# Performance work log

Hardware: AMD Instinct MI355X
Metric: run time of the kernel (lower is better)

Reference implementation:

```python
import jax, jax.numpy as jnp
import numpy as np

B, T, IN, H = 64, 2048, 512, 128
EPS = 1e-5


def mish(x):
    return x * jnp.tanh(jax.nn.softplus(x))


def layernorm(x, g, b):
    m = jnp.mean(x, axis=-1, keepdims=True)
    v = jnp.mean((x - m) ** 2, axis=-1, keepdims=True)
    return (x - m) / jnp.sqrt(v + EPS) * g + b


def gru_dir(x, Wih, Whh, bih, bhh, reverse):
    """One direction of a PyTorch-convention GRU layer.
    x: [B, T, D_in]; Wih: [3H, D_in]; Whh: [3H, H]. Returns ([B,T,H] outputs, [B,H] final h).
    Gate order matches torch: reset, update, new."""
    # Precompute all input projections once (hoists the big GEMM out of the scan)
    xp = jnp.einsum('bti,gi->tbg', x, Wih) + bih  # [T, B, 3H]
    h0 = jnp.zeros((x.shape[0], Whh.shape[1]), x.dtype)

    def step(h, xt):
        gh = h @ Whh.T + bhh
        xr, xz, xn = jnp.split(xt, 3, axis=-1)
        hr, hz, hn = jnp.split(gh, 3, axis=-1)
        r = jax.nn.sigmoid(xr + hr)
        z = jax.nn.sigmoid(xz + hz)
        n = jnp.tanh(xn + r * hn)
        h_new = (1.0 - z) * n + z * h
        return h_new, h_new

    hT, ys = jax.lax.scan(step, h0, xp, reverse=reverse)
    return jnp.transpose(ys, (1, 0, 2)), hT


def setup_inputs() -> dict:
    key = jax.random.key(0)
    ks = iter(jax.random.split(key, 32))
    s = 0.05

    def p(shape):
        return jax.random.normal(next(ks), shape, dtype=jnp.float32) * s

    inp = {'x': jax.random.normal(next(ks), (B, T, IN), dtype=jnp.float32)}
    # GRU layer 0 (input IN), layer 1 (input 2H from bidirectional concat); f/b directions
    for name, din in (('0f', IN), ('0b', IN), ('1f', 2 * H), ('1b', 2 * H)):
        inp['Wih' + name] = p((3 * H, din))
        inp['Whh' + name] = p((3 * H, H))
        inp['bih' + name] = p((3 * H,))
        inp['bhh' + name] = p((3 * H,))
    # post_gru LayerNorm
    inp['g1'] = jnp.ones((H,), jnp.float32)
    inp['be1'] = jnp.zeros((H,), jnp.float32)
    # decoder: Linear(H,H) -> Mish -> LayerNorm -> Linear(H,1)
    inp['W1'] = p((H, H))
    inp['b1'] = p((H,))
    inp['g2'] = jnp.ones((H,), jnp.float32)
    inp['be2'] = jnp.zeros((H,), jnp.float32)
    inp['W2'] = p((1, H))
    inp['b2'] = p((1,))
    return inp


def reference(x, Wih0f, Whh0f, bih0f, bhh0f, Wih0b, Whh0b, bih0b, bhh0b,
              Wih1f, Whh1f, bih1f, bhh1f, Wih1b, Whh1b, bih1b, bhh1b,
              g1, be1, W1, b1, g2, be2, W2, b2):
    # Layer 0, both directions
    of, _ = gru_dir(x, Wih0f, Whh0f, bih0f, bhh0f, reverse=False)
    ob, _ = gru_dir(x, Wih0b, Whh0b, bih0b, bhh0b, reverse=True)
    x1 = jnp.concatenate([of, ob], axis=-1)  # [B, T, 2H]; inter-layer dropout is identity in eval
    # Layer 1; keep final hidden states (h_n)
    _, hf = gru_dir(x1, Wih1f, Whh1f, bih1f, bhh1f, reverse=False)
    _, hb = gru_dir(x1, Wih1b, Whh1b, bih1b, bhh1b, reverse=True)
    h = hb  # h_n[-1]: last layer, backward direction (PyTorch h_n layout) -> [B, H]
    # post_gru: Mish -> LayerNorm -> AlphaDropout(eval=identity)
    h = layernorm(mish(h), g1, be1)
    # decoder: Linear -> Mish -> LayerNorm -> Linear
    h = layernorm(mish(h @ W1.T + b1), g2, be2)
    return h @ W2.T + b2  # [B, 1]
```

## Files before the change

### kernel.cpp

```cpp
#include <hip/hip_runtime.h>
#include <hip/hip_bf16.h>
#include <cstddef>

#define T_SEQ 2048
#define BATCH 64
#define H 128
#define EPS 1e-5f

typedef _Float16 half8_t __attribute__((ext_vector_type(8)));
typedef _Float16 half4_t __attribute__((ext_vector_type(4)));
typedef float floatx4 __attribute__((ext_vector_type(4)));

__device__ __forceinline__ float sigmoid_f(float x) {
    return __builtin_amdgcn_rcpf(1.0f + __expf(-x));
}
__device__ __forceinline__ float tanh_f(float x) {
    return fmaf(2.0f, __builtin_amdgcn_rcpf(1.0f + __expf(-2.0f * x)), -1.0f);
}
__device__ __forceinline__ float mish_f(float x) {
    float sp = (x > 15.0f) ? x : log1pf(__expf(x));
    return x * tanh_f(sp);
}


template<int K>
__global__ __launch_bounds__(256, 2)
void proj_kernel(const float* __restrict__ A, const float* __restrict__ W,
                 const float* __restrict__ bih, const float* __restrict__ bhh,
                 float* __restrict__ C)
{
    __shared__ float As[16][128];
    __shared__ float Ws[16][128];
    const int n0 = blockIdx.x * 128;
    const int m0 = blockIdx.y * 128;
    const int tid = threadIdx.x;
    const int tx = tid & 15;
    const int ty = tid >> 4;
    float acc[8][8];
    #pragma unroll
    for (int i = 0; i < 8; ++i)
        #pragma unroll
        for (int j = 0; j < 8; ++j) acc[i][j] = 0.0f;

    for (int k0 = 0; k0 < K; k0 += 16) {
        #pragma unroll
        for (int i = 0; i < 2; ++i) {
            const int f = tid + i * 256;
            const int r = f >> 2;
            const int kq = (f & 3) << 2;
            const int m = m0 + r;
            const size_t arow = (size_t)(m & 63) * T_SEQ + (m >> 6);
            const float4 av = *reinterpret_cast<const float4*>(&A[arow * K + k0 + kq]);
            As[kq + 0][r] = av.x; As[kq + 1][r] = av.y;
            As[kq + 2][r] = av.z; As[kq + 3][r] = av.w;
            const float4 wv = *reinterpret_cast<const float4*>(&W[(size_t)(n0 + r) * K + k0 + kq]);
            Ws[kq + 0][r] = wv.x; Ws[kq + 1][r] = wv.y;
            Ws[kq + 2][r] = wv.z; Ws[kq + 3][r] = wv.w;
        }
        __syncthreads();
        #pragma unroll
        for (int kk = 0; kk < 16; ++kk) {
            float a[8], b[8];
            *reinterpret_cast<float4*>(&a[0]) = *reinterpret_cast<const float4*>(&As[kk][ty * 8]);
            *reinterpret_cast<float4*>(&a[4]) = *reinterpret_cast<const float4*>(&As[kk][ty * 8 + 4]);
            *reinterpret_cast<float4*>(&b[0]) = *reinterpret_cast<const float4*>(&Ws[kk][tx * 8]);
            *reinterpret_cast<float4*>(&b[4]) = *reinterpret_cast<const float4*>(&Ws[kk][tx * 8 + 4]);
            #pragma unroll
            for (int i = 0; i < 8; ++i)
                #pragma unroll
                for (int j = 0; j < 8; ++j)
                    acc[i][j] = fmaf(a[i], b[j], acc[i][j]);
        }
        __syncthreads();
    }
    float bv[8];
    #pragma unroll
    for (int j = 0; j < 8; ++j) {
        const int col = n0 + tx * 8 + j;
        bv[j] = bih[col] + ((col < 256) ? bhh[col] : 0.0f);
    }
    const int cq0 = (n0 >> 2) + tx * 2;
    #pragma unroll
    for (int i = 0; i < 8; ++i) {
        const int m = m0 + ty * 8 + i;
        const int t = m >> 6, b = m & 63;
        const int gi = b >> 4, ni = b & 15;
        float* base = &C[(((size_t)t * 4 + gi) * 96 + cq0) * 64 + ni * 4];
        float4 o0, o1;
        o0.x = acc[i][0] + bv[0]; o0.y = acc[i][1] + bv[1];
        o0.z = acc[i][2] + bv[2]; o0.w = acc[i][3] + bv[3];
        o1.x = acc[i][4] + bv[4]; o1.y = acc[i][5] + bv[5];
        o1.z = acc[i][6] + bv[6]; o1.w = acc[i][7] + bv[7];
        *reinterpret_cast<float4*>(base) = o0;
        *reinterpret_cast<float4*>(base + 64) = o1;
    }
}

__device__ __forceinline__ int hoff(int n, int k) {
    return (n * 256 + k * 2) ^ ((n & 7) << 4);
}
#define LDS_BARRIER() asm volatile("s_waitcnt lgkmcnt(0)\n\ts_barrier" ::: "memory")

__global__ __launch_bounds__(512, 2)
void gru_scan8(const float* __restrict__ xpA, const float* __restrict__ xpB,
               const float* __restrict__ WA, const float* __restrict__ WB,
               const float* __restrict__ bA, const float* __restrict__ bB,
               int revA, int revB,
               float* __restrict__ seqout,
               float* __restrict__ hfin)
{
    const int tid = threadIdx.x;
    const int w = tid >> 6;
    const int l = tid & 63;
    const int n = l & 15;
    const int q = l >> 4;

    const int cid = blockIdx.x;
    const int dir = cid >> 2;
    const int g = cid & 3;

    const float* __restrict__ xp  = dir ? xpB : xpA;
    const float* __restrict__ Whh = dir ? WB : WA;
    const float* __restrict__ bhh = dir ? bB : bA;
    const int rev = dir ? revB : revA;

    __shared__ __align__(16) unsigned char hlds[2][4096];

    *reinterpret_cast<unsigned long long*>(&hlds[0][tid * 8]) = 0ull;

    half8_t wf[3][4];
    #pragma unroll
    for (int mi = 0; mi < 3; ++mi) {
        const float* wr = &Whh[(size_t)((mi * 8 + w) * 16 + n) * 128 + q * 8];
        #pragma unroll
        for (int kt = 0; kt < 4; ++kt) {
            half8_t hf;
            #pragma unroll
            for (int e = 0; e < 8; ++e) hf[e] = (_Float16)wr[kt * 32 + e];
            wf[mi][kt] = hf;
        }
    }

    const int batch = g * 16 + n;
    const floatx4 bN = *reinterpret_cast<const floatx4*>(&bhh[256 + w * 16 + q * 4]);
    floatx4 hp = {0.f, 0.f, 0.f, 0.f};

    const int t0 = rev ? (T_SEQ - 1) : 0;
    const int ts = rev ? -1 : 1;

    const float* xbase = xp + ((size_t)(g * 96 + w * 4 + q) * 16 + n) * 4;

#define XLOAD(S, T)                                                                 \
    do {                                                                            \
        const float* p_ = xbase + (size_t)(T) * 24576;                              \
        S[0] = *reinterpret_cast<const floatx4*>(p_);                               \
        S[1] = *reinterpret_cast<const floatx4*>(p_ + 2048);                        \
        S[2] = *reinterpret_cast<const floatx4*>(p_ + 4096);                        \
    } while (0)

    floatx4 XA[3], XB[3], XC[3], XD[3];
    XLOAD(XA, t0);
    XLOAD(XB, t0 + ts);
    XLOAD(XC, t0 + 2 * ts);

    __syncthreads();

#define GRU_STEP(RB, WB_, XS, TCUR)                                                 \
    do {                                                                            \
        half8_t bf0 = *reinterpret_cast<const half8_t*>(&hlds[RB][hoff(n, 0 * 32 + q * 8)]); \
        half8_t bf1 = *reinterpret_cast<const half8_t*>(&hlds[RB][hoff(n, 1 * 32 + q * 8)]); \
        half8_t bf2 = *reinterpret_cast<const half8_t*>(&hlds[RB][hoff(n, 2 * 32 + q * 8)]); \
        half8_t bf3 = *reinterpret_cast<const half8_t*>(&hlds[RB][hoff(n, 3 * 32 + q * 8)]); \
        floatx4 a0 = {0.f, 0.f, 0.f, 0.f};                                          \
        floatx4 a1 = {0.f, 0.f, 0.f, 0.f};                                          \
        floatx4 a2 = bN;                                                            \
        a0 = __builtin_amdgcn_mfma_f32_16x16x32_f16(wf[0][0], bf0, a0, 0, 0, 0);    \
        a1 = __builtin_amdgcn_mfma_f32_16x16x32_f16(wf[1][0], bf0, a1, 0, 0, 0);    \
        a2 = __builtin_amdgcn_mfma_f32_16x16x32_f16(wf[2][0], bf0, a2, 0, 0, 0);    \
        a0 = __builtin_amdgcn_mfma_f32_16x16x32_f16(wf[0][1], bf1, a0, 0, 0, 0);    \
        a1 = __builtin_amdgcn_mfma_f32_16x16x32_f16(wf[1][1], bf1, a1, 0, 0, 0);    \
        a2 = __builtin_amdgcn_mfma_f32_16x16x32_f16(wf[2][1], bf1, a2, 0, 0, 0);    \
        a0 = __builtin_amdgcn_mfma_f32_16x16x32_f16(wf[0][2], bf2, a0, 0, 0, 0);    \
        a1 = __builtin_amdgcn_mfma_f32_16x16x32_f16(wf[1][2], bf2, a1, 0, 0, 0);    \
        a2 = __builtin_amdgcn_mfma_f32_16x16x32_f16(wf[2][2], bf2, a2, 0, 0, 0);    \
        a0 = __builtin_amdgcn_mfma_f32_16x16x32_f16(wf[0][3], bf3, a0, 0, 0, 0);    \
        a1 = __builtin_amdgcn_mfma_f32_16x16x32_f16(wf[1][3], bf3, a1, 0, 0, 0);    \
        a2 = __builtin_amdgcn_mfma_f32_16x16x32_f16(wf[2][3], bf3, a2, 0, 0, 0);    \
        floatx4 hnew;                                                               \
        half4_t hh;                                                                 \
        _Pragma("unroll")                                                           \
        for (int rr = 0; rr < 4; ++rr) {                                            \
            const float rg = sigmoid_f(a0[rr] + XS[0][rr]);                         \
            const float zg = sigmoid_f(a1[rr] + XS[1][rr]);                         \
            const float nn = tanh_f(XS[2][rr] + rg * a2[rr]);                       \
            const float hv = fmaf(zg, hp[rr] - nn, nn);                             \
            hnew[rr] = hv;                                                          \
            hh[rr] = (_Float16)hv;                                                  \
        }                                                                           \
        hp = hnew;                                                                  \
        *reinterpret_cast<half4_t*>(&hlds[WB_][hoff(n, w * 16 + q * 4)]) = hh;      \
        if (seqout)                                                                 \
            *reinterpret_cast<floatx4*>(                                            \
                &seqout[((size_t)batch * T_SEQ + (TCUR)) * 256 + dir * 128 +        \
                        w * 16 + q * 4]) = hnew;                                    \
        LDS_BARRIER();                                                              \
    } while (0)

#define CLAMP_T(v) ((v) < 0 ? 0 : ((v) > T_SEQ - 1 ? T_SEQ - 1 : (v)))

    int t = t0;
    for (int it = 0; it < T_SEQ / 4; ++it) {
        { const int tl = CLAMP_T(t + 3 * ts); XLOAD(XD, tl); }
        GRU_STEP(0, 1, XA, t); t += ts;
        { const int tl = CLAMP_T(t + 3 * ts); XLOAD(XA, tl); }
        GRU_STEP(1, 0, XB, t); t += ts;
        { const int tl = CLAMP_T(t + 3 * ts); XLOAD(XB, tl); }
        GRU_STEP(0, 1, XC, t); t += ts;
        { const int tl = CLAMP_T(t + 3 * ts); XLOAD(XC, tl); }
        GRU_STEP(1, 0, XD, t); t += ts;
    }
#undef GRU_STEP
#undef XLOAD
#undef CLAMP_T

    if (hfin)
        *reinterpret_cast<floatx4*>(&hfin[(size_t)batch * 128 + w * 16 + q * 4]) = hp;
}

__device__ __forceinline__ float block_sum128(float v, float* red) {
    #pragma unroll
    for (int o = 32; o > 0; o >>= 1) v += __shfl_down(v, o);
    const int w = threadIdx.x >> 6;
    if ((threadIdx.x & 63) == 0) red[w] = v;
    __syncthreads();
    const float s = red[0] + red[1];
    __syncthreads();
    return s;
}

__global__ __launch_bounds__(128, 1)
void decoder_kernel(const float* __restrict__ hb,
                    const float* __restrict__ g1, const float* __restrict__ be1,
                    const float* __restrict__ W1, const float* __restrict__ b1,
                    const float* __restrict__ g2, const float* __restrict__ be2,
                    const float* __restrict__ W2, const float* __restrict__ b2,
                    float* __restrict__ out)
{
    const int b = blockIdx.x;
    const int j = threadIdx.x;
    __shared__ float buf[H];
    __shared__ float red[2];

    const float m = mish_f(hb[(size_t)b * H + j]);
    const float mean = block_sum128(m, red) * (1.0f / H);
    const float d = m - mean;
    const float var = block_sum128(d * d, red) * (1.0f / H);
    const float y = d * rsqrtf(var + EPS) * g1[j] + be1[j];
    buf[j] = y;
    __syncthreads();

    float acc = b1[j];
    #pragma unroll
    for (int k = 0; k < H; k += 4) {
        const float4 wv = *reinterpret_cast<const float4*>(&W1[(size_t)j * H + k]);
        const float4 yv = *reinterpret_cast<const float4*>(&buf[k]);
        acc += wv.x * yv.x + wv.y * yv.y + wv.z * yv.z + wv.w * yv.w;
    }
    const float m2 = mish_f(acc);
    const float mean2 = block_sum128(m2, red) * (1.0f / H);
    const float d2 = m2 - mean2;
    const float var2 = block_sum128(d2 * d2, red) * (1.0f / H);
    const float y2 = d2 * rsqrtf(var2 + EPS) * g2[j] + be2[j];

    const float p = W2[j] * y2;
    const float s = block_sum128(p, red);
    if (j == 0) out[b] = s + b2[0];
}

extern "C" void kernel_launch(void* const* d_in, const int* in_sizes, int n_in,
                              void* d_out, int out_size, void* d_ws, size_t ws_size,
                              hipStream_t stream)
{
    (void)in_sizes; (void)n_in; (void)out_size; (void)ws_size;
    const float* x     = (const float*)d_in[0];
    const float* Wih0f = (const float*)d_in[1];
    const float* Whh0f = (const float*)d_in[2];
    const float* bih0f = (const float*)d_in[3];
    const float* bhh0f = (const float*)d_in[4];
    const float* Wih0b = (const float*)d_in[5];
    const float* Whh0b = (const float*)d_in[6];
    const float* bih0b = (const float*)d_in[7];
    const float* bhh0b = (const float*)d_in[8];
    const float* Wih1b = (const float*)d_in[13];
    const float* Whh1b = (const float*)d_in[14];
    const float* bih1b = (const float*)d_in[15];
    const float* bhh1b = (const float*)d_in[16];
    const float* g1  = (const float*)d_in[17];
    const float* be1 = (const float*)d_in[18];
    const float* W1  = (const float*)d_in[19];
    const float* b1  = (const float*)d_in[20];
    const float* g2  = (const float*)d_in[21];
    const float* be2 = (const float*)d_in[22];
    const float* W2  = (const float*)d_in[23];
    const float* b2  = (const float*)d_in[24];
    float* out = (float*)d_out;

    float* ws = (float*)d_ws;
    const size_t XP_ELEMS = (size_t)T_SEQ * BATCH * 384;
    const size_t X1_ELEMS = (size_t)BATCH * T_SEQ * 256;
    float* xp0f = ws;
    float* xp0b = xp0f + XP_ELEMS;
    float* x1   = xp0b + XP_ELEMS;
    float* hbuf = x1 + X1_ELEMS;
    float* xp1b = xp0f;

    const dim3 pgrid(3, 1024);
    proj_kernel<512><<<pgrid, 256, 0, stream>>>(x, Wih0f, bih0f, bhh0f, xp0f);
    proj_kernel<512><<<pgrid, 256, 0, stream>>>(x, Wih0b, bih0b, bhh0b, xp0b);
    gru_scan8<<<dim3(8), 512, 0, stream>>>(xp0f, xp0b, Whh0f, Whh0b, bhh0f, bhh0b,
                                           0, 1, x1, nullptr);
    proj_kernel<256><<<pgrid, 256, 0, stream>>>(x1, Wih1b, bih1b, bhh1b, xp1b);
    gru_scan8<<<dim3(4), 512, 0, stream>>>(xp1b, xp1b, Whh1b, Whh1b, bhh1b, bhh1b,
                                           1, 1, nullptr, hbuf);
    decoder_kernel<<<64, 128, 0, stream>>>(hbuf, g1, be1, W1, b1, g2, be2, W2, b2, out);
}
```

Before: 4.896 ms.

## Replace FP32 projection GEMM with FP16 MFMA kernel and double-buffered LDS

Rewrites the input-projection GEMM to convert inputs and weights to fp16 in shared memory and compute with 16x16x32 MFMA instructions, accumulating in fp32. Global loads for the next K tile are issued before the current tile's MFMAs and staged into a second LDS buffer, so memory latency overlaps with compute. This targets the scalar-FMA cost of the three projection GEMMs. The trade-off is reduced input precision, since activations and weights are rounded to fp16 before the multiply.

```diff
diff --git a/kernel.cpp b/kernel.cpp
--- a/kernel.cpp
+++ b/kernel.cpp
@@ -25,74 +25,107 @@
 
 template<int K>
 __global__ __launch_bounds__(256, 2)
-void proj_kernel(const float* __restrict__ A, const float* __restrict__ W,
-                 const float* __restrict__ bih, const float* __restrict__ bhh,
-                 float* __restrict__ C)
+void proj_mfma(const float* __restrict__ A, const float* __restrict__ W,
+               const float* __restrict__ bih, const float* __restrict__ bhh,
+               float* __restrict__ C)
 {
-    __shared__ float As[16][128];
-    __shared__ float Ws[16][128];
+    constexpr int NKT = K / 32;
+    __shared__ _Float16 Ws[2][128][40];
+    __shared__ _Float16 Xs[2][128][40];
+
+    const int tid = threadIdx.x;
+    const int w = tid >> 6, l = tid & 63;
+    const int lm = l & 15, q = l >> 4;
+    const int wm = (w & 1) * 64, wn = (w >> 1) * 64;
     const int n0 = blockIdx.x * 128;
     const int m0 = blockIdx.y * 128;
-    const int tid = threadIdx.x;
-    const int tx = tid & 15;
-    const int ty = tid >> 4;
-    float acc[8][8];
-    #pragma unroll
-    for (int i = 0; i < 8; ++i)
-        #pragma unroll
-        for (int j = 0; j < 8; ++j) acc[i][j] = 0.0f;
-
-    for (int k0 = 0; k0 < K; k0 += 16) {
-        #pragma unroll
-        for (int i = 0; i < 2; ++i) {
-            const int f = tid + i * 256;
-            const int r = f >> 2;
-            const int kq = (f & 3) << 2;
-            const int m = m0 + r;
-            const size_t arow = (size_t)(m & 63) * T_SEQ + (m >> 6);
-            const float4 av = *reinterpret_cast<const float4*>(&A[arow * K + k0 + kq]);
-            As[kq + 0][r] = av.x; As[kq + 1][r] = av.y;
-            As[kq + 2][r] = av.z; As[kq + 3][r] = av.w;
-            const float4 wv = *reinterpret_cast<const float4*>(&W[(size_t)(n0 + r) * K + k0 + kq]);
-            Ws[kq + 0][r] = wv.x; Ws[kq + 1][r] = wv.y;
-            Ws[kq + 2][r] = wv.z; Ws[kq + 3][r] = wv.w;
+
+    const int sr = tid >> 1;
+    const int sk = (tid & 1) * 16;
+    const int sm = m0 + sr;
+    const float* xrow = A + ((size_t)(sm & 63) * T_SEQ + (sm >> 6)) * K + sk;
+    const float* wrow = W + (size_t)(n0 + sr) * K + sk;
+
+    floatx4 acc[4][4];
+    #pragma unroll
+    for (int i = 0; i < 4; ++i)
+        #pragma unroll
+        for (int j = 0; j < 4; ++j) acc[i][j] = floatx4{0.f, 0.f, 0.f, 0.f};
+
+    floatx4 bv[4];
+    #pragma unroll
+    for (int nf = 0; nf < 4; ++nf) {
+        const int nc = n0 + wn + nf * 16 + q * 4;
+        floatx4 b = *reinterpret_cast<const floatx4*>(&bih[nc]);
+        if (nc < 256) b += *reinterpret_cast<const floatx4*>(&bhh[nc]);
+        bv[nf] = b;
+    }
+
+    floatx4 lx[4], lw[4];
+
+#define STORE_STAGE(B)                                                          \
+    do {                                                                        \
+        half8_t h0, h1, g0, g1;                                                 \
+        _Pragma("unroll")                                                       \
+        for (int e = 0; e < 4; ++e) {                                           \
+            h0[e] = (_Float16)lx[0][e]; h0[4 + e] = (_Float16)lx[1][e];         \
+            h1[e] = (_Float16)lx[2][e]; h1[4 + e] = (_Float16)lx[3][e];         \
+            g0[e] = (_Float16)lw[0][e]; g0[4 + e] = (_Float16)lw[1][e];         \
+            g1[e] = (_Float16)lw[2][e]; g1[4 + e] = (_Float16)lw[3][e];         \
+        }                                                                       \
+        *reinterpret_cast<half8_t*>(&Xs[B][sr][sk])     = h0;                   \
+        *reinterpret_cast<half8_t*>(&Xs[B][sr][sk + 8]) = h1;                   \
+        *reinterpret_cast<half8_t*>(&Ws[B][sr][sk])     = g0;                   \
+        *reinterpret_cast<half8_t*>(&Ws[B][sr][sk + 8]) = g1;                   \
+    } while (0)
+
+    #pragma unroll
+    for (int i = 0; i < 4; ++i) {
+        lx[i] = *reinterpret_cast<const floatx4*>(xrow + i * 4);
+        lw[i] = *reinterpret_cast<const floatx4*>(wrow + i * 4);
+    }
+    STORE_STAGE(0);
+    __syncthreads();
+
+    int buf = 0;
+    for (int kt = 0; kt < NKT; ++kt) {
+        if (kt + 1 < NKT) {
+            #pragma unroll
+            for (int i = 0; i < 4; ++i) {
+                lx[i] = *reinterpret_cast<const floatx4*>(xrow + (kt + 1) * 32 + i * 4);
+                lw[i] = *reinterpret_cast<const floatx4*>(wrow + (kt + 1) * 32 + i * 4);
+            }
         }
+        half8_t af[4], bf[4];
+        #pragma unroll
+        for (int f = 0; f < 4; ++f) {
+            af[f] = *reinterpret_cast<const half8_t*>(&Ws[buf][wn + f * 16 + lm][q * 8]);
+            bf[f] = *reinterpret_cast<const half8_t*>(&Xs[buf][wm + f * 16 + lm][q * 8]);
+        }
+        #pragma unroll
+        for (int nf = 0; nf < 4; ++nf)
+            #pragma unroll
+            for (int mf = 0; mf < 4; ++mf)
+                acc[nf][mf] = __builtin_amdgcn_mfma_f32_16x16x32_f16(
+                    af[nf], bf[mf], acc[nf][mf], 0, 0, 0);
+        if (kt + 1 < NKT) STORE_STAGE(buf ^ 1);
         __syncthreads();
-        #pragma unroll
-        for (int kk = 0; kk < 16; ++kk) {
-            float a[8], b[8];
-            *reinterpret_cast<float4*>(&a[0]) = *reinterpret_cast<const float4*>(&As[kk][ty * 8]);
-            *reinterpret_cast<float4*>(&a[4]) = *reinterpret_cast<const float4*>(&As[kk][ty * 8 + 4]);
-            *reinterpret_cast<float4*>(&b[0]) = *reinterpret_cast<const float4*>(&Ws[kk][tx * 8]);
-            *reinterpret_cast<float4*>(&b[4]) = *reinterpret_cast<const float4*>(&Ws[kk][tx * 8 + 4]);
-            #pragma unroll
-            for (int i = 0; i < 8; ++i)
-                #pragma unroll
-                for (int j = 0; j < 8; ++j)
-                    acc[i][j] = fmaf(a[i], b[j], acc[i][j]);
+        buf ^= 1;
+    }
+#undef STORE_STAGE
+
+    #pragma unroll
+    for (int nf = 0; nf < 4; ++nf) {
+        const int nc = n0 + wn + nf * 16 + q * 4;
+        const int cq = nc >> 2;
+        #pragma unroll
+        for (int mf = 0; mf < 4; ++mf) {
+            const int m = m0 + wm + mf * 16 + lm;
+            const int t = m >> 6, g = (m >> 4) & 3, nb = m & 15;
+            const floatx4 o = acc[nf][mf] + bv[nf];
+            *reinterpret_cast<floatx4*>(
+                &C[(((size_t)t * 4 + g) * 96 + cq) * 64 + nb * 4]) = o;
         }
-        __syncthreads();
-    }
-    float bv[8];
-    #pragma unroll
-    for (int j = 0; j < 8; ++j) {
-        const int col = n0 + tx * 8 + j;
-        bv[j] = bih[col] + ((col < 256) ? bhh[col] : 0.0f);
-    }
-    const int cq0 = (n0 >> 2) + tx * 2;
-    #pragma unroll
-    for (int i = 0; i < 8; ++i) {
-        const int m = m0 + ty * 8 + i;
-        const int t = m >> 6, b = m & 63;
-        const int gi = b >> 4, ni = b & 15;
-        float* base = &C[(((size_t)t * 4 + gi) * 96 + cq0) * 64 + ni * 4];
-        float4 o0, o1;
-        o0.x = acc[i][0] + bv[0]; o0.y = acc[i][1] + bv[1];
-        o0.z = acc[i][2] + bv[2]; o0.w = acc[i][3] + bv[3];
-        o1.x = acc[i][4] + bv[4]; o1.y = acc[i][5] + bv[5];
-        o1.z = acc[i][6] + bv[6]; o1.w = acc[i][7] + bv[7];
-        *reinterpret_cast<float4*>(base) = o0;
-        *reinterpret_cast<float4*>(base + 64) = o1;
     }
 }
 
@@ -315,11 +348,11 @@
     float* xp1b = xp0f;
 
     const dim3 pgrid(3, 1024);
-    proj_kernel<512><<<pgrid, 256, 0, stream>>>(x, Wih0f, bih0f, bhh0f, xp0f);
-    proj_kernel<512><<<pgrid, 256, 0, stream>>>(x, Wih0b, bih0b, bhh0b, xp0b);
+    proj_mfma<512><<<pgrid, 256, 0, stream>>>(x, Wih0f, bih0f, bhh0f, xp0f);
+    proj_mfma<512><<<pgrid, 256, 0, stream>>>(x, Wih0b, bih0b, bhh0b, xp0b);
     gru_scan8<<<dim3(8), 512, 0, stream>>>(xp0f, xp0b, Whh0f, Whh0b, bhh0f, bhh0b,
                                            0, 1, x1, nullptr);
-    proj_kernel<256><<<pgrid, 256, 0, stream>>>(x1, Wih1b, bih1b, bhh1b, xp1b);
+    proj_mfma<256><<<pgrid, 256, 0, stream>>>(x1, Wih1b, bih1b, bhh1b, xp1b);
     gru_scan8<<<dim3(4), 512, 0, stream>>>(xp1b, xp1b, Whh1b, Whh1b, bhh1b, bhh1b,
                                            1, 1, nullptr, hbuf);
     decoder_kernel<<<64, 128, 0, stream>>>(hbuf, g1, be1, W1, b1, g2, be2, W2, b2, out);
```

Measured after the change: 3.936 ms. 1.24x faster.
